# Kernel optimization log

Measured on AMD Instinct MI355X. Metric: run time of the kernel, lower is better.

The kernel has to match this reference:

```python
import jax, jax.numpy as jnp
import numpy as np

ROI = 5            # roi_size hardcoded in RPFeatureExtractor(..., roi_size=5)
NUM_CLASSES = 80
MEM_SIZE = 1024


def _roi_align(rp, b, boxes):
    # rp: [B,C,H,W]; b: [N] int batch index; boxes: [N,4] xyxy in feature-map coords.
    # torchvision roi_align semantics, spatial_scale=1, aligned=False.
    # Here roi extents are <=1 (normalized boxes), so roi_w/h clamp to 1.0 and the
    # adaptive sampling_ratio = ceil(1/ROI) = 1 sample per bin (bin-center bilinear).
    B, C, H, W = rp.shape
    rpT = jnp.transpose(rp, (0, 2, 3, 1))  # [B,H,W,C]
    x1, y1, x2, y2 = boxes[:, 0], boxes[:, 1], boxes[:, 2], boxes[:, 3]
    roi_w = jnp.maximum(x2 - x1, 1.0)
    roi_h = jnp.maximum(y2 - y1, 1.0)
    g = jnp.arange(ROI, dtype=rp.dtype) + 0.5
    sx = x1[:, None] + g[None, :] * (roi_w / ROI)[:, None]   # [N,ROI]
    sy = y1[:, None] + g[None, :] * (roi_h / ROI)[:, None]   # [N,ROI]
    N = boxes.shape[0]
    x = jnp.broadcast_to(sx[:, None, :], (N, ROI, ROI))
    y = jnp.broadcast_to(sy[:, :, None], (N, ROI, ROI))
    invalid = (y < -1.0) | (y > H) | (x < -1.0) | (x > W)
    y = jnp.maximum(y, 0.0)
    x = jnp.maximum(x, 0.0)
    yl = jnp.floor(y).astype(jnp.int32)
    xl = jnp.floor(x).astype(jnp.int32)
    y = jnp.where(yl >= H - 1, jnp.asarray(H - 1, rp.dtype), y)
    x = jnp.where(xl >= W - 1, jnp.asarray(W - 1, rp.dtype), x)
    yl = jnp.minimum(yl, H - 1)
    xl = jnp.minimum(xl, W - 1)
    yh = jnp.minimum(yl + 1, H - 1)
    xh = jnp.minimum(xl + 1, W - 1)
    ly = (y - yl.astype(rp.dtype))[..., None]
    lx = (x - xl.astype(rp.dtype))[..., None]
    hy, hx = 1.0 - ly, 1.0 - lx
    bb = b[:, None, None]
    v = (rpT[bb, yl, xl] * hy * hx + rpT[bb, yl, xh] * hy * lx
         + rpT[bb, yh, xl] * ly * hx + rpT[bb, yh, xh] * ly * lx)  # [N,ROI,ROI,C]
    v = jnp.where(invalid[..., None], jnp.asarray(0.0, rp.dtype), v)
    # torch output is [N,C,ROI,ROI] flattened -> transpose before reshape
    return jnp.transpose(v, (0, 3, 1, 2)).reshape(N, -1)


def _project_and_normalize(feats, w1, b1, w2, b2):
    h = jax.nn.relu(feats @ w1.T + b1)
    f = h @ w2.T + b2
    f = f + 1e-8                                   # source adds eps before normalize
    n = jnp.linalg.norm(f, axis=1, keepdims=True)
    return f / jnp.maximum(n, 1e-12)               # F.normalize semantics


def _update_memory(feat_norm, cls, memory_bank, memory_count, class_freq):
    feats_d = jax.lax.stop_gradient(feat_norm)     # .detach() in source
    onehot = (cls[:, None] == jnp.arange(NUM_CLASSES)[None, :]).astype(jnp.int32)
    occ = jnp.cumsum(onehot, axis=0) - onehot      # exclusive per-class rank
    occ_i = jnp.take_along_axis(occ, cls[:, None].astype(jnp.int32), axis=1)[:, 0]
    pos = (memory_count[cls] + occ_i) % MEM_SIZE
    flat = cls.astype(jnp.int32) * MEM_SIZE + pos
    dim = memory_bank.shape[-1]
    mb = memory_bank.reshape(NUM_CLASSES * MEM_SIZE, dim).at[flat].set(feats_d)
    mb = mb.reshape(NUM_CLASSES, MEM_SIZE, dim)
    per_cls = jnp.sum(onehot, axis=0)
    count_new = memory_count + per_cls
    freq_new = class_freq + per_cls.astype(class_freq.dtype)
    total = jnp.sum(freq_new)
    prob = jnp.clip(freq_new / total, 1e-8, None)
    cw = 1.0 / jnp.sqrt(prob + 1e-8)
    cw = cw / cw.mean()
    return mb, count_new, freq_new, cw


def setup_inputs() -> dict:
    key = jax.random.key(0)
    ks = jax.random.split(key, 8)
    B, C, H, W, N = 16, 256, 128, 128, 512
    enc, hid, dim = C * ROI * ROI, 2048, 256
    return {
        "rp_features": jax.random.normal(ks[0], (B, C, H, W), jnp.float32),
        "batch_idx": jax.random.randint(ks[1], (N,), 0, B, jnp.int32),
        "cls": jax.random.randint(ks[2], (N,), 0, NUM_CLASSES, jnp.int32),
        "bboxes": jax.random.uniform(ks[3], (N, 4), jnp.float32),  # normalized xywh
        "img_h": 640,
        "img_w": 640,
        "w1": jax.random.normal(ks[4], (hid, enc), jnp.float32) * 0.02,
        "b1": jnp.zeros((hid,), jnp.float32),
        "w2": jax.random.normal(ks[5], (dim, hid), jnp.float32) * 0.02,
        "b2": jnp.zeros((dim,), jnp.float32),
        "memory_bank": jnp.zeros((NUM_CLASSES, MEM_SIZE, dim), jnp.float32),
        "memory_count": jnp.zeros((NUM_CLASSES,), jnp.int32),
        "class_freq": jnp.zeros((NUM_CLASSES,), jnp.float32),
    }


def reference(rp_features, batch_idx, cls, bboxes, img_h, img_w,
              w1, b1, w2, b2, memory_bank, memory_count, class_freq):
    # xywh (normalized) -> xyxy; source scales by img_size then divides it back
    # inside extract_roi_features, so boxes end up in [0,1] feature-map coords.
    cx, cy, w, h = bboxes[:, 0], bboxes[:, 1], bboxes[:, 2], bboxes[:, 3]
    boxes = jnp.stack([cx - w / 2, cy - h / 2, cx + w / 2, cy + h / 2], axis=1)
    # valid_mask (x2>x1 & y2>y1) always true here since w,h > 0 by construction.
    feats = _roi_align(rp_features, batch_idx, boxes)           # [N, C*25]
    feat_norm = _project_and_normalize(feats, w1, b1, w2, b2)   # [N, 256]
    mb, count_new, freq_new, cw = _update_memory(
        feat_norm, cls, memory_bank, memory_count, class_freq)
    return feat_norm, mb, count_new, cw
```

## Files before the change

### kernel.cpp

```cpp
#include <hip/hip_runtime.h>

#define NBOX 512
#define ENC 6400
#define HID 2048
#define DIM 256
#define NCLS 80
#define MEMSZ 1024
#define Bm 16
#define Cc 256
#define Hh 128
#define Ww 128

typedef __attribute__((ext_vector_type(8))) short bf16x8;
typedef __attribute__((ext_vector_type(4))) float f32x4;

__device__ __forceinline__ ushort f2bf(float x) {
  union { float f; unsigned u; } v;
  v.f = x;
  const unsigned r = v.u + 0x7fffu + ((v.u >> 16) & 1u);
  return (ushort)(r >> 16);
}

__global__ __launch_bounds__(256) void roi_scan_copy_kernel(
    const float* __restrict__ rp, const int* __restrict__ bidx,
    const float* __restrict__ bboxes, ushort* __restrict__ feats, int N,
    const int* __restrict__ cls, const int* __restrict__ mcount,
    const float* __restrict__ cfreq, int* __restrict__ pos,
    float* __restrict__ outCNT, float* __restrict__ outCW,
    const float4* __restrict__ csrc, float4* __restrict__ cdst, int cn4) {
  const int n = blockIdx.x;
  if (n > N) {
    const int nb = (int)gridDim.x - (N + 1);
    const int cb = n - (N + 1);
    for (int i = cb * 256 + (int)threadIdx.x; i < cn4; i += nb * 256) cdst[i] = csrc[i];
    return;
  }
  if (n == N) {
    __shared__ int scls[NBOX];
    __shared__ float sf[NCLS], sc[NCLS];
    __shared__ float s_tot, s_mean;
    const int t = threadIdx.x;
    if (t < 128) *(int4*)&scls[t * 4] = *(const int4*)&cls[t * 4];
    __syncthreads();
    if (t < NCLS) {
      int cnt = 0;
      const int base = mcount[t];
      for (int i = 0; i < N; ++i) {
        if (scls[i] == t) { pos[i] = (base + cnt) % MEMSZ; ++cnt; }
      }
      outCNT[t] = (float)(base + cnt);
      sf[t] = cfreq[t] + (float)cnt;
    }
    __syncthreads();
    if (t == 0) {
      float s = 0.0f;
      for (int i = 0; i < NCLS; ++i) s += sf[i];
      s_tot = s;
    }
    __syncthreads();
    if (t < NCLS) sc[t] = 1.0f / sqrtf(fmaxf(sf[t] / s_tot, 1e-8f) + 1e-8f);
    __syncthreads();
    if (t == 0) {
      float s = 0.0f;
      for (int i = 0; i < NCLS; ++i) s += sc[i];
      s_mean = s / (float)NCLS;
    }
    __syncthreads();
    if (t < NCLS) outCW[t] = sc[t] / s_mean;
    return;
  }
  const int b = bidx[n];
  const float cx = bboxes[n * 4 + 0], cy = bboxes[n * 4 + 1];
  const float bw = bboxes[n * 4 + 2], bh = bboxes[n * 4 + 3];
  const float x1 = cx - bw * 0.5f, y1 = cy - bh * 0.5f;
  const float x2 = cx + bw * 0.5f, y2 = cy + bh * 0.5f;
  const float roi_w = fmaxf(x2 - x1, 1.0f), roi_h = fmaxf(y2 - y1, 1.0f);
  const float stx = roi_w / 5.0f, sty = roi_h / 5.0f;
  for (int j4 = threadIdx.x; j4 < ENC / 4; j4 += 256) {
    ushort4 o;
    float ov[4];
#pragma unroll
    for (int e = 0; e < 4; ++e) {
      const int j = j4 * 4 + e;
      const int c = j / 25, p = j % 25, gy = p / 5, gx = p % 5;
      const float sx = x1 + ((float)gx + 0.5f) * stx;
      const float sy = y1 + ((float)gy + 0.5f) * sty;
      const bool invalid = (sy < -1.0f) || (sy > (float)Hh) || (sx < -1.0f) || (sx > (float)Ww);
      float v = 0.0f;
      if (!invalid) {
        float y = fmaxf(sy, 0.0f), x = fmaxf(sx, 0.0f);
        int yl = (int)floorf(y), xl = (int)floorf(x);
        if (yl >= Hh - 1) y = (float)(Hh - 1);
        if (xl >= Ww - 1) x = (float)(Ww - 1);
        yl = min(yl, Hh - 1);
        xl = min(xl, Ww - 1);
        const int yh = min(yl + 1, Hh - 1), xh = min(xl + 1, Ww - 1);
        const float ly = y - (float)yl, lx = x - (float)xl;
        const float hy = 1.0f - ly, hx = 1.0f - lx;
        const float* base = rp + ((long)(b * Cc + c) << 14);
        const float v00 = base[(yl << 7) + xl];
        const float v01 = base[(yl << 7) + xh];
        const float v10 = base[(yh << 7) + xl];
        const float v11 = base[(yh << 7) + xh];
        v = v00 * hy * hx + v01 * hy * lx + v10 * ly * hx + v11 * ly * lx;
      }
      ov[e] = v;
    }
    o.x = f2bf(ov[0]); o.y = f2bf(ov[1]); o.z = f2bf(ov[2]); o.w = f2bf(ov[3]);
    *(ushort4*)(feats + (long)n * ENC + j4 * 4) = o;
  }
}

__global__ __launch_bounds__(256) void gemm1_splitk(
    const ushort* __restrict__ A, const float* __restrict__ B,
    float* __restrict__ P) {
  const int tid = threadIdx.x;
  __shared__ ushort lds[2][16384];
  const int lane = tid & 63;
  const int wave = tid >> 6;
  const int wr = wave >> 1, wc = wave & 1;
  const int m0 = blockIdx.y * 128, n0 = blockIdx.x * 128;
  const long kz = (long)blockIdx.z * 1280;

  f32x4 acc[4][4];
#pragma unroll
  for (int i = 0; i < 4; ++i)
#pragma unroll
    for (int j = 0; j < 4; ++j) acc[i][j] = (f32x4)0.0f;

  int4 aR[4];
  float4 bR[8];

  auto G_load = [&](int kt) {
#pragma unroll
    for (int p = 0; p < 4; ++p) {
      const int cid = tid + p * 256;
      const int row = cid >> 3, c = cid & 7;
      aR[p] = *(const int4*)(A + (long)(m0 + row) * ENC + kz + kt + c * 8);
      const float* bp = B + (long)(n0 + row) * ENC + kz + kt + c * 8;
      bR[p * 2] = *(const float4*)bp;
      bR[p * 2 + 1] = *(const float4*)(bp + 4);
    }
  };
  auto L_store = [&](int buf) {
    ushort* Ab = &lds[buf][0];
    ushort* Bb = &lds[buf][8192];
#pragma unroll
    for (int p = 0; p < 4; ++p) {
      const int cid = tid + p * 256;
      const int row = cid >> 3, c = (cid & 7) ^ (row & 7);
      *(int4*)&Ab[row * 64 + c * 8] = aR[p];
      ushort4 lo, hi;
      lo.x = f2bf(bR[p * 2].x); lo.y = f2bf(bR[p * 2].y);
      lo.z = f2bf(bR[p * 2].z); lo.w = f2bf(bR[p * 2].w);
      hi.x = f2bf(bR[p * 2 + 1].x); hi.y = f2bf(bR[p * 2 + 1].y);
      hi.z = f2bf(bR[p * 2 + 1].z); hi.w = f2bf(bR[p * 2 + 1].w);
      *(ushort4*)&Bb[row * 64 + c * 8] = lo;
      *(ushort4*)&Bb[row * 64 + c * 8 + 4] = hi;
    }
  };

  const int lr = lane & 15;
  const int g = lane >> 4;
  constexpr int NT = 20;

  G_load(0);
  L_store(0);
  __syncthreads();
  for (int t = 0; t < NT; ++t) {
    const int cur = t & 1;
    if (t + 1 < NT) G_load((t + 1) * 64);
    const ushort* Ab = &lds[cur][0];
    const ushort* Bb = &lds[cur][8192];
#pragma unroll
    for (int h0 = 0; h0 < 2; ++h0) {
      bf16x8 a[4], b[4];
#pragma unroll
      for (int i = 0; i < 4; ++i) {
        const int row = wr * 64 + i * 16 + lr;
        a[i] = *(const bf16x8*)&Ab[row * 64 + ((h0 * 4 + g) ^ (row & 7)) * 8];
      }
#pragma unroll
      for (int j = 0; j < 4; ++j) {
        const int row = wc * 64 + j * 16 + lr;
        b[j] = *(const bf16x8*)&Bb[row * 64 + ((h0 * 4 + g) ^ (row & 7)) * 8];
      }
#pragma unroll
      for (int i = 0; i < 4; ++i)
#pragma unroll
        for (int j = 0; j < 4; ++j)
          acc[i][j] = __builtin_amdgcn_mfma_f32_16x16x32_bf16(a[i], b[j], acc[i][j], 0, 0, 0);
    }
    if (t + 1 < NT) L_store(cur ^ 1);
    __syncthreads();
  }

  float* Pp = P + (long)blockIdx.z * NBOX * HID;
  const int r0 = m0 + wr * 64 + ((lane >> 4) << 2);
  const int c0 = n0 + wc * 64 + lr;
#pragma unroll
  for (int i = 0; i < 4; ++i)
#pragma unroll
    for (int j = 0; j < 4; ++j)
#pragma unroll
      for (int r = 0; r < 4; ++r)
        Pp[(long)(r0 + i * 16 + r) * HID + c0 + j * 16] = acc[i][j][r];
}

__global__ __launch_bounds__(256) void reduce_bias_relu_bf16(
    const float* __restrict__ P, const float* __restrict__ bias,
    ushort* __restrict__ out, int MN, int Ncols, int Z) {
  const int e = (blockIdx.x * 256 + threadIdx.x) * 4;
  if (e >= MN) return;
  float4 s = *(const float4*)(P + e);
  for (int z = 1; z < Z; ++z) {
    const float4 t = *(const float4*)(P + (long)z * MN + e);
    s.x += t.x; s.y += t.y; s.z += t.z; s.w += t.w;
  }
  const float4 bb = *(const float4*)(bias + (e & (Ncols - 1)));
  ushort4 o;
  o.x = f2bf(fmaxf(s.x + bb.x, 0.0f));
  o.y = f2bf(fmaxf(s.y + bb.y, 0.0f));
  o.z = f2bf(fmaxf(s.z + bb.z, 0.0f));
  o.w = f2bf(fmaxf(s.w + bb.w, 0.0f));
  *(ushort4*)(out + e) = o;
}

template <int BM, int BN, int WM, int WN, int TM, int TN>
__global__ __launch_bounds__(WM * WN * 64) void gemm_bf16_nt(
    const ushort* __restrict__ A, const float* __restrict__ B,
    float* __restrict__ P, int M, int N, int K, int kchunk) {
  constexpr int THREADS = WM * WN * 64;
  const int tid = threadIdx.x;
  constexpr int CA = BM * 4 / THREADS;
  constexpr int CB = BN * 8 / THREADS;
  __shared__ ushort As[2][BM][40];
  __shared__ ushort Bs[2][BN][40];
  const int lane = tid & 63;
  const int wave = tid >> 6;
  const int wr = wave / WN, wc = wave % WN;
  const int m0 = blockIdx.y * BM, n0 = blockIdx.x * BN;
  const long kz = (long)blockIdx.z * kchunk;

  f32x4 acc[TM][TN];
#pragma unroll
  for (int i = 0; i < TM; ++i)
#pragma unroll
    for (int j = 0; j < TN; ++j) acc[i][j] = (f32x4)0.0f;

  int4 areg[CA];
  float4 breg[CB];

  auto loadt = [&](int kt) {
#pragma unroll
    for (int i = 0; i < CA; ++i) {
      const int f = tid + i * THREADS;
      areg[i] = *(const int4*)(A + (long)(m0 + (f >> 2)) * K + kz + kt + (f & 3) * 8);
    }
#pragma unroll
    for (int i = 0; i < CB; ++i) {
      const int f = tid + i * THREADS;
      breg[i] = *(const float4*)(B + (long)(n0 + (f >> 3)) * K + kz + kt + (f & 7) * 4);
    }
  };
  auto storet = [&](int buf) {
#pragma unroll
    for (int i = 0; i < CA; ++i) {
      const int f = tid + i * THREADS;
      *(int4*)&As[buf][f >> 2][(f & 3) * 8] = areg[i];
    }
#pragma unroll
    for (int i = 0; i < CB; ++i) {
      const int f = tid + i * THREADS;
      const float4 bv = breg[i];
      ushort4 o;
      o.x = f2bf(bv.x); o.y = f2bf(bv.y); o.z = f2bf(bv.z); o.w = f2bf(bv.w);
      *(ushort4*)&Bs[buf][f >> 3][(f & 7) * 4] = o;
    }
  };

  const int lrow = lane & 15;
  const int kb = (lane >> 4) * 8;
  const int NT = kchunk / 32;

  loadt(0);
  storet(0);
  __syncthreads();
  for (int t = 0; t < NT; ++t) {
    const int cur = t & 1;
    if (t + 1 < NT) loadt((t + 1) * 32);
    bf16x8 a[TM], b[TN];
#pragma unroll
    for (int i = 0; i < TM; ++i)
      a[i] = *(const bf16x8*)&As[cur][wr * (TM * 16) + i * 16 + lrow][kb];
#pragma unroll
    for (int j = 0; j < TN; ++j)
      b[j] = *(const bf16x8*)&Bs[cur][wc * (TN * 16) + j * 16 + lrow][kb];
#pragma unroll
    for (int i = 0; i < TM; ++i)
#pragma unroll
      for (int j = 0; j < TN; ++j)
        acc[i][j] = __builtin_amdgcn_mfma_f32_16x16x32_bf16(a[i], b[j], acc[i][j], 0, 0, 0);
    if (t + 1 < NT) storet(cur ^ 1);
    __syncthreads();
  }

  float* Pp = P + (long)blockIdx.z * M * N;
  const int r0 = m0 + wr * (TM * 16) + ((lane >> 4) << 2);
  const int c0 = n0 + wc * (TN * 16) + lrow;
#pragma unroll
  for (int i = 0; i < TM; ++i)
#pragma unroll
    for (int j = 0; j < TN; ++j)
#pragma unroll
      for (int r = 0; r < 4; ++r)
        Pp[(long)(r0 + i * 16 + r) * N + c0 + j * 16] = acc[i][j][r];
}

__global__ __launch_bounds__(256) void reduce_norm_scatter(
    const float* __restrict__ P, const float* __restrict__ b2,
    float* __restrict__ outFN, float* __restrict__ outMB,
    const int* __restrict__ cls, const int* __restrict__ pos, int M, int Z) {
  const int m = blockIdx.x, d = threadIdx.x;
  float f = 0.0f;
  for (int z = 0; z < Z; ++z) f += P[((long)z * M + m) * DIM + d];
  f += b2[d] + 1e-8f;
  float ss = f * f;
#pragma unroll
  for (int o = 32; o > 0; o >>= 1) ss += __shfl_xor(ss, o, 64);
  __shared__ float sred[4];
  if ((d & 63) == 0) sred[d >> 6] = ss;
  __syncthreads();
  const float tot = sred[0] + sred[1] + sred[2] + sred[3];
  const float nrm = fmaxf(sqrtf(tot), 1e-12f);
  const float r = f / nrm;
  outFN[(long)m * DIM + d] = r;
  outMB[((long)cls[m] * MEMSZ + pos[m]) * DIM + d] = r;
}

extern "C" void kernel_launch(void* const* d_in, const int* in_sizes, int n_in,
                              void* d_out, int out_size, void* d_ws, size_t ws_size,
                              hipStream_t stream) {
  const float* rp = (const float*)d_in[0];
  const int* bidx = (const int*)d_in[1];
  const int* cls = (const int*)d_in[2];
  const float* bboxes = (const float*)d_in[3];
  const float* w1 = (const float*)d_in[6];
  const float* b1 = (const float*)d_in[7];
  const float* w2 = (const float*)d_in[8];
  const float* b2 = (const float*)d_in[9];
  const float* mbank = (const float*)d_in[10];
  const int* mcount = (const int*)d_in[11];
  const float* cfreq = (const float*)d_in[12];
  const int N = in_sizes[1];

  char* ws = (char*)d_ws;
  ushort* feats = (ushort*)ws;
  float* P1 = (float*)(ws + 6553600);
  ushort* h = (ushort*)(ws + 6553600 + 20971520);
  int* pos = (int*)(ws + 6553600 + 20971520 + 2097152);
  float* P2 = P1;

  float* outFN = (float*)d_out;
  float* outMB = outFN + (long)NBOX * DIM;
  float* outCNT = outMB + (long)NCLS * MEMSZ * DIM;
  float* outCW = outCNT + NCLS;

  roi_scan_copy_kernel<<<N + 1 + 1536, 256, 0, stream>>>(
      rp, bidx, bboxes, feats, N, cls, mcount, cfreq, pos, outCNT, outCW,
      (const float4*)mbank, (float4*)outMB, NCLS * MEMSZ * DIM / 4);

  gemm1_splitk<<<dim3(HID / 128, NBOX / 128, 5), 256, 0, stream>>>(feats, w1, P1);
  reduce_bias_relu_bf16<<<NBOX * HID / 4 / 256, 256, 0, stream>>>(
      P1, b1, h, NBOX * HID, HID, 5);

  gemm_bf16_nt<128, 64, 2, 2, 4, 2><<<dim3(DIM / 64, NBOX / 128, 8), 256, 0, stream>>>(
      h, w2, P2, NBOX, DIM, HID, HID / 8);

  reduce_norm_scatter<<<NBOX, 256, 0, stream>>>(P2, b2, outFN, outMB, cls, pos, NBOX, 8);
}
```

Measured before the change: 128.3 us.

## Pre-convert w1 to bf16 in the prologue kernel and stage GEMM1 tiles via global_load_lds

The first kernel's copy blocks are split in two groups. One group copies the memory bank with 4x unrolled float4 moves, and the other converts the fp32 w1 weights to bf16 in workspace. GEMM1 then reads bf16 B directly and loads both A and B tiles straight into LDS with global_load_lds, so there is no register staging or per-tile conversion. The second GEMM's tile width also changes from 64 to 32 columns. The trade-off is an extra full write and re-read of w1 in bf16, done every call, plus heavier work in the prologue kernel. The new LDS staging also depends on the direct-to-LDS load layout matching the existing swizzled reads.

Measured after the change: 135.7 us. +5.8%, slower.

```diff
diff --git a/kernel.cpp b/kernel.cpp
--- a/kernel.cpp
+++ b/kernel.cpp
@@ -21,18 +21,42 @@
   return (ushort)(r >> 16);
 }
 
+__device__ __forceinline__ void glds16(const ushort* g, ushort* l) {
+  __builtin_amdgcn_global_load_lds((const __attribute__((address_space(1))) void*)g,
+                                   (__attribute__((address_space(3))) void*)l, 16, 0, 0);
+}
+
 __global__ __launch_bounds__(256) void roi_scan_copy_kernel(
     const float* __restrict__ rp, const int* __restrict__ bidx,
     const float* __restrict__ bboxes, ushort* __restrict__ feats, int N,
     const int* __restrict__ cls, const int* __restrict__ mcount,
     const float* __restrict__ cfreq, int* __restrict__ pos,
     float* __restrict__ outCNT, float* __restrict__ outCW,
-    const float4* __restrict__ csrc, float4* __restrict__ cdst, int cn4) {
+    const float4* __restrict__ csrc, float4* __restrict__ cdst, int cn4,
+    const float* __restrict__ w1f, ushort* __restrict__ w1b) {
   const int n = blockIdx.x;
   if (n > N) {
-    const int nb = (int)gridDim.x - (N + 1);
     const int cb = n - (N + 1);
-    for (int i = cb * 256 + (int)threadIdx.x; i < cn4; i += nb * 256) cdst[i] = csrc[i];
+    if (cb < 1152) {
+      const int base = (cb * 256 + (int)threadIdx.x) * 4;
+      const int stride = 1152 * 256 * 4;
+      for (int i = base; i + 3 < cn4; i += stride) {
+        const float4 a0 = csrc[i], a1 = csrc[i + 1], a2 = csrc[i + 2], a3 = csrc[i + 3];
+        cdst[i] = a0; cdst[i + 1] = a1; cdst[i + 2] = a2; cdst[i + 3] = a3;
+      }
+    } else {
+      const int wt = (cb - 1152) * 256 + (int)threadIdx.x;
+      const int nchunk = HID * ENC / 8;
+      for (int i = wt; i < nchunk; i += 384 * 256) {
+        const float4 f0 = *(const float4*)(w1f + (long)i * 8);
+        const float4 f1 = *(const float4*)(w1f + (long)i * 8 + 4);
+        ushort4 lo, hi;
+        lo.x = f2bf(f0.x); lo.y = f2bf(f0.y); lo.z = f2bf(f0.z); lo.w = f2bf(f0.w);
+        hi.x = f2bf(f1.x); hi.y = f2bf(f1.y); hi.z = f2bf(f1.z); hi.w = f2bf(f1.w);
+        *(ushort4*)(w1b + (long)i * 8) = lo;
+        *(ushort4*)(w1b + (long)i * 8 + 4) = hi;
+      }
+    }
     return;
   }
   if (n == N) {
@@ -112,12 +136,11 @@
 }
 
 __global__ __launch_bounds__(256) void gemm1_splitk(
-    const ushort* __restrict__ A, const float* __restrict__ B,
+    const ushort* __restrict__ A, const ushort* __restrict__ Bb16,
     float* __restrict__ P) {
+  __shared__ ushort lds[2][16384];
   const int tid = threadIdx.x;
-  __shared__ ushort lds[2][16384];
-  const int lane = tid & 63;
-  const int wave = tid >> 6;
+  const int lane = tid & 63, wave = tid >> 6;
   const int wr = wave >> 1, wc = wave & 1;
   const int m0 = blockIdx.y * 128, n0 = blockIdx.x * 128;
   const long kz = (long)blockIdx.z * 1280;
@@ -128,35 +151,17 @@
 #pragma unroll
     for (int j = 0; j < 4; ++j) acc[i][j] = (f32x4)0.0f;
 
-  int4 aR[4];
-  float4 bR[8];
-
-  auto G_load = [&](int kt) {
-#pragma unroll
-    for (int p = 0; p < 4; ++p) {
-      const int cid = tid + p * 256;
-      const int row = cid >> 3, c = cid & 7;
-      aR[p] = *(const int4*)(A + (long)(m0 + row) * ENC + kz + kt + c * 8);
-      const float* bp = B + (long)(n0 + row) * ENC + kz + kt + c * 8;
-      bR[p * 2] = *(const float4*)bp;
-      bR[p * 2 + 1] = *(const float4*)(bp + 4);
-    }
-  };
-  auto L_store = [&](int buf) {
+  auto stage = [&](int buf, int kt) {
     ushort* Ab = &lds[buf][0];
-    ushort* Bb = &lds[buf][8192];
-#pragma unroll
-    for (int p = 0; p < 4; ++p) {
-      const int cid = tid + p * 256;
-      const int row = cid >> 3, c = (cid & 7) ^ (row & 7);
-      *(int4*)&Ab[row * 64 + c * 8] = aR[p];
-      ushort4 lo, hi;
-      lo.x = f2bf(bR[p * 2].x); lo.y = f2bf(bR[p * 2].y);
-      lo.z = f2bf(bR[p * 2].z); lo.w = f2bf(bR[p * 2].w);
-      hi.x = f2bf(bR[p * 2 + 1].x); hi.y = f2bf(bR[p * 2 + 1].y);
-      hi.z = f2bf(bR[p * 2 + 1].z); hi.w = f2bf(bR[p * 2 + 1].w);
-      *(ushort4*)&Bb[row * 64 + c * 8] = lo;
-      *(ushort4*)&Bb[row * 64 + c * 8 + 4] = hi;
+    ushort* Bbl = &lds[buf][8192];
+#pragma unroll
+    for (int q = 0; q < 4; ++q) {
+      const int seg = wave * 4 + q;
+      const int row = seg * 8 + (lane >> 3);
+      const int cc = (lane & 7) ^ (row & 7);
+      const long goff = (long)row * ENC + kz + kt + cc * 8;
+      glds16(A + (long)m0 * ENC + goff, &Ab[seg * 512]);
+      glds16(Bb16 + (long)n0 * ENC + goff, &Bbl[seg * 512]);
     }
   };
 
@@ -164,14 +169,13 @@
   const int g = lane >> 4;
   constexpr int NT = 20;
 
-  G_load(0);
-  L_store(0);
+  stage(0, 0);
   __syncthreads();
   for (int t = 0; t < NT; ++t) {
     const int cur = t & 1;
-    if (t + 1 < NT) G_load((t + 1) * 64);
+    if (t + 1 < NT) stage(cur ^ 1, (t + 1) * 64);
     const ushort* Ab = &lds[cur][0];
-    const ushort* Bb = &lds[cur][8192];
+    const ushort* Bbl = &lds[cur][8192];
 #pragma unroll
     for (int h0 = 0; h0 < 2; ++h0) {
       bf16x8 a[4], b[4];
@@ -183,7 +187,7 @@
 #pragma unroll
       for (int j = 0; j < 4; ++j) {
         const int row = wc * 64 + j * 16 + lr;
-        b[j] = *(const bf16x8*)&Bb[row * 64 + ((h0 * 4 + g) ^ (row & 7)) * 8];
+        b[j] = *(const bf16x8*)&Bbl[row * 64 + ((h0 * 4 + g) ^ (row & 7)) * 8];
       }
 #pragma unroll
       for (int i = 0; i < 4; ++i)
@@ -191,7 +195,6 @@
         for (int j = 0; j < 4; ++j)
           acc[i][j] = __builtin_amdgcn_mfma_f32_16x16x32_bf16(a[i], b[j], acc[i][j], 0, 0, 0);
     }
-    if (t + 1 < NT) L_store(cur ^ 1);
     __syncthreads();
   }
 
@@ -359,6 +362,7 @@
   float* P1 = (float*)(ws + 6553600);
   ushort* h = (ushort*)(ws + 6553600 + 20971520);
   int* pos = (int*)(ws + 6553600 + 20971520 + 2097152);
+  ushort* w1b = (ushort*)(ws + 6553600 + 20971520 + 2097152 + 2048);
   float* P2 = P1;
 
   float* outFN = (float*)d_out;
@@ -368,13 +372,13 @@
 
   roi_scan_copy_kernel<<<N + 1 + 1536, 256, 0, stream>>>(
       rp, bidx, bboxes, feats, N, cls, mcount, cfreq, pos, outCNT, outCW,
-      (const float4*)mbank, (float4*)outMB, NCLS * MEMSZ * DIM / 4);
-
-  gemm1_splitk<<<dim3(HID / 128, NBOX / 128, 5), 256, 0, stream>>>(feats, w1, P1);
+      (const float4*)mbank, (float4*)outMB, NCLS * MEMSZ * DIM / 4, w1, w1b);
+
+  gemm1_splitk<<<dim3(HID / 128, NBOX / 128, 5), 256, 0, stream>>>(feats, w1b, P1);
   reduce_bias_relu_bf16<<<NBOX * HID / 4 / 256, 256, 0, stream>>>(
       P1, b1, h, NBOX * HID, HID, 5);
 
-  gemm_bf16_nt<128, 64, 2, 2, 4, 2><<<dim3(DIM / 64, NBOX / 128, 8), 256, 0, stream>>>(
+  gemm_bf16_nt<128, 32, 2, 2, 4, 1><<<dim3(DIM / 32, NBOX / 128, 8), 256, 0, stream>>>(
       h, w2, P2, NBOX, DIM, HID, HID / 8);
 
   reduce_norm_scatter<<<NBOX, 256, 0, stream>>>(P2, b2, outFN, outMB, cls, pos, NBOX, 8);
```

## Retile gemm1 to 256x128 blocks with 512 threads, BK=32, split-K 10

Applied to the files above, without the earlier changes.

The first projection GEMM now uses 256x128 output tiles computed by 8 waves (512 threads) with a 32-wide K step, a new XOR swizzle, and 10-way split-K instead of 5. Each block converts the fp32 W1 tile to bf16 once and reuses it across twice as many A rows, which halves the redundant W1 reads and conversions. Block count stays at 320 while per-thread register staging shrinks. The cost is a doubled split-K partial buffer (more workspace and more reduction traffic) and a barrier every 32 K elements.

Measured after the change: 148.6 us. 15.8% more time.

```diff
diff --git a/kernel.cpp b/kernel.cpp
--- a/kernel.cpp
+++ b/kernel.cpp
@@ -20,6 +20,8 @@
   const unsigned r = v.u + 0x7fffu + ((v.u >> 16) & 1u);
   return (ushort)(r >> 16);
 }
+
+__device__ __forceinline__ int swz(int r) { return (r ^ (r >> 1)) & 3; }
 
 __global__ __launch_bounds__(256) void roi_scan_copy_kernel(
     const float* __restrict__ rp, const int* __restrict__ bidx,
@@ -111,16 +113,15 @@
   }
 }
 
-__global__ __launch_bounds__(256) void gemm1_splitk(
+__global__ __launch_bounds__(512) void gemm1_splitk(
     const ushort* __restrict__ A, const float* __restrict__ B,
     float* __restrict__ P) {
+  __shared__ ushort lds[2][12288];
   const int tid = threadIdx.x;
-  __shared__ ushort lds[2][16384];
-  const int lane = tid & 63;
-  const int wave = tid >> 6;
+  const int lane = tid & 63, wave = tid >> 6;
   const int wr = wave >> 1, wc = wave & 1;
-  const int m0 = blockIdx.y * 128, n0 = blockIdx.x * 128;
-  const long kz = (long)blockIdx.z * 1280;
+  const int m0 = blockIdx.y * 256, n0 = blockIdx.x * 128;
+  const long kz = (long)blockIdx.z * 640;
 
   f32x4 acc[4][4];
 #pragma unroll
@@ -128,35 +129,40 @@
 #pragma unroll
     for (int j = 0; j < 4; ++j) acc[i][j] = (f32x4)0.0f;
 
-  int4 aR[4];
-  float4 bR[8];
+  int4 aR[2];
+  float4 bR[2];
 
   auto G_load = [&](int kt) {
 #pragma unroll
-    for (int p = 0; p < 4; ++p) {
-      const int cid = tid + p * 256;
-      const int row = cid >> 3, c = cid & 7;
-      aR[p] = *(const int4*)(A + (long)(m0 + row) * ENC + kz + kt + c * 8);
-      const float* bp = B + (long)(n0 + row) * ENC + kz + kt + c * 8;
-      bR[p * 2] = *(const float4*)bp;
-      bR[p * 2 + 1] = *(const float4*)(bp + 4);
+    for (int p = 0; p < 2; ++p) {
+      const int cid = tid + p * 512;
+      const int row = cid >> 2, c4 = cid & 3;
+      aR[p] = *(const int4*)(A + (long)(m0 + row) * ENC + kz + kt + c4 * 8);
+    }
+    {
+      const int row = tid >> 2, c4 = tid & 3;
+      const float* bp = B + (long)(n0 + row) * ENC + kz + kt + c4 * 8;
+      bR[0] = *(const float4*)bp;
+      bR[1] = *(const float4*)(bp + 4);
     }
   };
   auto L_store = [&](int buf) {
     ushort* Ab = &lds[buf][0];
     ushort* Bb = &lds[buf][8192];
 #pragma unroll
-    for (int p = 0; p < 4; ++p) {
-      const int cid = tid + p * 256;
-      const int row = cid >> 3, c = (cid & 7) ^ (row & 7);
-      *(int4*)&Ab[row * 64 + c * 8] = aR[p];
-      ushort4 lo, hi;
-      lo.x = f2bf(bR[p * 2].x); lo.y = f2bf(bR[p * 2].y);
-      lo.z = f2bf(bR[p * 2].z); lo.w = f2bf(bR[p * 2].w);
-      hi.x = f2bf(bR[p * 2 + 1].x); hi.y = f2bf(bR[p * 2 + 1].y);
-      hi.z = f2bf(bR[p * 2 + 1].z); hi.w = f2bf(bR[p * 2 + 1].w);
-      *(ushort4*)&Bb[row * 64 + c * 8] = lo;
-      *(ushort4*)&Bb[row * 64 + c * 8 + 4] = hi;
+    for (int p = 0; p < 2; ++p) {
+      const int cid = tid + p * 512;
+      const int row = cid >> 2, c4 = cid & 3;
+      *(int4*)&Ab[row * 32 + (c4 ^ swz(row)) * 8] = aR[p];
+    }
+    {
+      const int row = tid >> 2, c4 = tid & 3;
+      ushort tmp[8];
+      tmp[0] = f2bf(bR[0].x); tmp[1] = f2bf(bR[0].y);
+      tmp[2] = f2bf(bR[0].z); tmp[3] = f2bf(bR[0].w);
+      tmp[4] = f2bf(bR[1].x); tmp[5] = f2bf(bR[1].y);
+      tmp[6] = f2bf(bR[1].z); tmp[7] = f2bf(bR[1].w);
+      *(int4*)&Bb[row * 32 + (c4 ^ swz(row)) * 8] = *(int4*)tmp;
     }
   };
 
@@ -169,34 +175,31 @@
   __syncthreads();
   for (int t = 0; t < NT; ++t) {
     const int cur = t & 1;
-    if (t + 1 < NT) G_load((t + 1) * 64);
+    if (t + 1 < NT) G_load((t + 1) * 32);
     const ushort* Ab = &lds[cur][0];
     const ushort* Bb = &lds[cur][8192];
-#pragma unroll
-    for (int h0 = 0; h0 < 2; ++h0) {
-      bf16x8 a[4], b[4];
-#pragma unroll
-      for (int i = 0; i < 4; ++i) {
-        const int row = wr * 64 + i * 16 + lr;
-        a[i] = *(const bf16x8*)&Ab[row * 64 + ((h0 * 4 + g) ^ (row & 7)) * 8];
-      }
-#pragma unroll
-      for (int j = 0; j < 4; ++j) {
-        const int row = wc * 64 + j * 16 + lr;
-        b[j] = *(const bf16x8*)&Bb[row * 64 + ((h0 * 4 + g) ^ (row & 7)) * 8];
-      }
-#pragma unroll
-      for (int i = 0; i < 4; ++i)
-#pragma unroll
-        for (int j = 0; j < 4; ++j)
-          acc[i][j] = __builtin_amdgcn_mfma_f32_16x16x32_bf16(a[i], b[j], acc[i][j], 0, 0, 0);
-    }
+    bf16x8 a[4], b[4];
+#pragma unroll
+    for (int i = 0; i < 4; ++i) {
+      const int row = wr * 64 + i * 16 + lr;
+      a[i] = *(const bf16x8*)&Ab[row * 32 + (g ^ swz(row)) * 8];
+    }
+#pragma unroll
+    for (int j = 0; j < 4; ++j) {
+      const int row = wc * 64 + j * 16 + lr;
+      b[j] = *(const bf16x8*)&Bb[row * 32 + (g ^ swz(row)) * 8];
+    }
+#pragma unroll
+    for (int i = 0; i < 4; ++i)
+#pragma unroll
+      for (int j = 0; j < 4; ++j)
+        acc[i][j] = __builtin_amdgcn_mfma_f32_16x16x32_bf16(a[i], b[j], acc[i][j], 0, 0, 0);
     if (t + 1 < NT) L_store(cur ^ 1);
     __syncthreads();
   }
 
   float* Pp = P + (long)blockIdx.z * NBOX * HID;
-  const int r0 = m0 + wr * 64 + ((lane >> 4) << 2);
+  const int r0 = m0 + wr * 64 + (g << 2);
   const int c0 = n0 + wc * 64 + lr;
 #pragma unroll
   for (int i = 0; i < 4; ++i)
@@ -357,8 +360,8 @@
   char* ws = (char*)d_ws;
   ushort* feats = (ushort*)ws;
   float* P1 = (float*)(ws + 6553600);
-  ushort* h = (ushort*)(ws + 6553600 + 20971520);
-  int* pos = (int*)(ws + 6553600 + 20971520 + 2097152);
+  ushort* h = (ushort*)(ws + 6553600 + 41943040);
+  int* pos = (int*)(ws + 6553600 + 41943040 + 2097152);
   float* P2 = P1;
 
   float* outFN = (float*)d_out;
@@ -370,9 +373,10 @@
       rp, bidx, bboxes, feats, N, cls, mcount, cfreq, pos, outCNT, outCW,
       (const float4*)mbank, (float4*)outMB, NCLS * MEMSZ * DIM / 4);
 
-  gemm1_splitk<<<dim3(HID / 128, NBOX / 128, 5), 256, 0, stream>>>(feats, w1, P1);
+  gemm1_splitk<<<dim3(HID / 128, NBOX / 256, 10), 512, 0, stream>>>(feats, w1, P1);
+
   reduce_bias_relu_bf16<<<NBOX * HID / 4 / 256, 256, 0, stream>>>(
-      P1, b1, h, NBOX * HID, HID, 5);
+      P1, b1, h, NBOX * HID, HID, 10);
 
   gemm_bf16_nt<128, 64, 2, 2, 4, 2><<<dim3(DIM / 64, NBOX / 128, 8), 256, 0, stream>>>(
       h, w2, P2, NBOX, DIM, HID, HID / 8);
```
